# Performance work log

Measured on AMD Instinct MI355X. Metric: run time of the kernel, lower is better.

## Reference

```python
import jax, jax.numpy as jnp
import numpy as np

B, T, D, U_DIM = 256, 512, 256, 256


def setup_inputs() -> dict:
    key = jax.random.key(0)
    k_x, k_len, k_w, k_u, k_b = jax.random.split(key, 5)
    codes = jax.random.normal(k_x, (B, T, D), dtype=jnp.float32)
    # random valid lengths; zero the tail so Masking(mask_value=0) kicks in
    lengths = jax.random.randint(k_len, (B,), T // 2, T + 1)
    valid = (jnp.arange(T)[None, :] < lengths[:, None]).astype(jnp.float32)
    codes = codes * valid[:, :, None]
    # Keras GRU params (reset_after=True): kernel, recurrent_kernel, bias[2, 3U]
    s_in = 1.0 / np.sqrt(D)
    s_rec = 1.0 / np.sqrt(U_DIM)
    W = jax.random.uniform(k_w, (D, 3 * U_DIM), jnp.float32, -s_in, s_in)
    Uk = jax.random.uniform(k_u, (U_DIM, 3 * U_DIM), jnp.float32, -s_rec, s_rec)
    b = jax.random.uniform(k_b, (2, 3 * U_DIM), jnp.float32, -s_rec, s_rec)
    return {"codes": codes, "W": W, "Uk": Uk, "b": b}


def _gru_scan(codes, W, Uk, b):
    units = Uk.shape[0]
    # Masking(mask_value=0): timestep is masked if ALL features equal 0
    mask = jnp.any(codes != 0.0, axis=-1)  # [B, T] bool
    # Precompute input projections for all timesteps: [B, T, 3U]
    mat_x = jnp.einsum("btd,dk->btk", codes, W) + b[0]
    xs = (jnp.swapaxes(mat_x, 0, 1), jnp.swapaxes(mask, 0, 1))  # time-major
    h0 = jnp.zeros((codes.shape[0], units), dtype=codes.dtype)

    def step(h, inp):
        mx_t, m_t = inp  # [B, 3U], [B]
        mh_t = h @ Uk + b[1]  # [B, 3U]
        xz, xr, xh = jnp.split(mx_t, 3, axis=-1)
        hz, hr, hh = jnp.split(mh_t, 3, axis=-1)
        z = jax.nn.sigmoid(xz + hz)
        r = jax.nn.sigmoid(xr + hr)
        h_cand = jnp.tanh(xh + r * hh)
        h_new = z * h + (1.0 - z) * h_cand
        h_out = jnp.where(m_t[:, None], h_new, h)  # carry state on masked steps
        return h_out, None

    h_final, _ = jax.lax.scan(step, h0, xs)
    return h_final  # [B, units]


def reference(codes, W, Uk, b):
    return _gru_scan(codes, W, Uk, b)
```

## Files before the change

### kernel.cpp

```cpp
#include <hip/hip_runtime.h>
#include <hip/hip_bf16.h>
#include <cstdint>
#include <cstddef>

#define Bb 256
#define Tt 512
#define Dd 256
#define Uu 256
#define NJ 768

#define WS_MASK  1024
#define WS_UKP   132096
#define WS_MATX  525312

typedef _Float16 h2 __attribute__((ext_vector_type(2)));
typedef short short8 __attribute__((ext_vector_type(8)));
typedef float f32x4 __attribute__((ext_vector_type(4)));

#if defined(__has_builtin)
#if __has_builtin(__builtin_amdgcn_fdot2)
#define HAVE_FDOT2 1
#endif
#endif

__device__ __forceinline__ unsigned int pack2(float a, float b) {
    h2 v;
    v.x = (_Float16)a;
    v.y = (_Float16)b;
    return __builtin_bit_cast(unsigned int, v);
}

__device__ __forceinline__ float dot2_acc(unsigned int u, unsigned int hv, float acc) {
    h2 a = __builtin_bit_cast(h2, u);
    h2 b = __builtin_bit_cast(h2, hv);
#ifdef HAVE_FDOT2
    return __builtin_amdgcn_fdot2(a, b, acc, false);
#else
    return acc + (float)a.x * (float)b.x + (float)a.y * (float)b.y;
#endif
}

__device__ __forceinline__ void bfsplit(float x, unsigned short& h, unsigned short& l) {
    unsigned u = __builtin_bit_cast(unsigned, x);
    h = (unsigned short)(u >> 16);
    float hf = __builtin_bit_cast(float, u & 0xFFFF0000u);
    float lf = x - hf;
    l = (unsigned short)(__builtin_bit_cast(unsigned, lf) >> 16);
}

union PK8 { unsigned short s[8]; uint4 v; };

__global__ void zero_len_kernel(int* __restrict__ len) {
    if (threadIdx.x < Bb) len[threadIdx.x] = 0;
}

__global__ void mask_len_kernel(const float* __restrict__ codes,
                                unsigned char* __restrict__ mask,
                                int* __restrict__ len) {
    const int wave = threadIdx.x >> 6;
    const int lane = threadIdx.x & 63;
    const long long row = (long long)blockIdx.x * 4 + wave;
    const float4* p = reinterpret_cast<const float4*>(codes + row * Dd);
    float4 v = p[lane];
    bool nz = (v.x != 0.f) || (v.y != 0.f) || (v.z != 0.f) || (v.w != 0.f);
    unsigned long long ball = __ballot(nz);
    if (lane == 0) {
        int b = (int)(row >> 9);
        int t = (int)(row & 511);
        unsigned char m = (ball != 0ull) ? 1 : 0;
        mask[row] = m;
        if (m) atomicMax(&len[b], t + 1);
    }
}

__global__ void uk_convert_kernel(const float* __restrict__ Uk,
                                  unsigned int* __restrict__ ukp) {
    int idx = blockIdx.x * 256 + threadIdx.x;
    int col = idx & 255;
    int kp = (idx >> 8) & 127;
    int g = idx >> 15;
    float a = Uk[(size_t)(2 * kp) * NJ + (g << 8) + col];
    float b = Uk[(size_t)(2 * kp + 1) * NJ + (g << 8) + col];
    ukp[idx] = pack2(a, b);
}

__global__ __launch_bounds__(256, 2)
void matx_gemm_mfma(const float* __restrict__ codes,
                    const float* __restrict__ W,
                    const float* __restrict__ b0,
                    float* __restrict__ matx,
                    int t0, int ctShift) {
    __shared__ uint4 AH[1024], AL[1024], BH[1024], BL[1024];
    const int tid = threadIdx.x;
    const int w = tid >> 6, lane = tid & 63;
    const int rbase = blockIdx.x * 128, cbase = blockIdx.y * 128;
    const int ctMask = (1 << ctShift) - 1;

    f32x4 acc[4][4];
#pragma unroll
    for (int i = 0; i < 4; ++i)
#pragma unroll
        for (int j = 0; j < 4; ++j) acc[i][j] = (f32x4){0.f, 0.f, 0.f, 0.f};

    const int cB = tid & 127, kqB = tid >> 7;

    for (int kt = 0; kt < 4; ++kt) {
        const int k0 = kt * 64;
#pragma unroll
        for (int u = 0; u < 4; ++u) {
            int L = u * 256 + tid;
            int r = L >> 3, o = L & 7;
            int gr = rbase + r;
            size_t g = (size_t)(gr >> ctShift) * Tt + (size_t)(t0 + (gr & ctMask));
            const float* cp = codes + g * Dd + k0 + (o << 3);
            float4 f0 = *reinterpret_cast<const float4*>(cp);
            float4 f1 = *reinterpret_cast<const float4*>(cp + 4);
            float e[8] = {f0.x, f0.y, f0.z, f0.w, f1.x, f1.y, f1.z, f1.w};
            PK8 hp, lp;
#pragma unroll
            for (int i = 0; i < 8; ++i) bfsplit(e[i], hp.s[i], lp.s[i]);
            int idx = (((o >> 2) * 8 + (r >> 4)) << 6) + ((r & 15) | ((o & 3) << 4));
            AH[idx] = hp.v;
            AL[idx] = lp.v;
        }
        {
            PK8 ph[4], pl[4];
#pragma unroll
            for (int j = 0; j < 32; ++j) {
                float v = W[(size_t)(k0 + kqB * 32 + j) * NJ + cbase + cB];
                bfsplit(v, ph[j >> 3].s[j & 7], pl[j >> 3].s[j & 7]);
            }
#pragma unroll
            for (int o2 = 0; o2 < 4; ++o2) {
                int idx = ((kqB * 8 + (cB >> 4)) << 6) + ((cB & 15) | (o2 << 4));
                BH[idx] = ph[o2].v;
                BL[idx] = pl[o2].v;
            }
        }
        __syncthreads();
        const int mbase = (w & 1) * 4, nbase = (w >> 1) * 4;
#pragma unroll
        for (int ki = 0; ki < 2; ++ki) {
            short8 ah[4], al2[4], bh[4], bl2[4];
#pragma unroll
            for (int x = 0; x < 4; ++x) {
                ah[x]  = *reinterpret_cast<const short8*>(&AH[((ki * 8 + mbase + x) << 6) + lane]);
                al2[x] = *reinterpret_cast<const short8*>(&AL[((ki * 8 + mbase + x) << 6) + lane]);
                bh[x]  = *reinterpret_cast<const short8*>(&BH[((ki * 8 + nbase + x) << 6) + lane]);
                bl2[x] = *reinterpret_cast<const short8*>(&BL[((ki * 8 + nbase + x) << 6) + lane]);
            }
#pragma unroll
            for (int mi = 0; mi < 4; ++mi)
#pragma unroll
                for (int ni = 0; ni < 4; ++ni) {
                    acc[mi][ni] = __builtin_amdgcn_mfma_f32_16x16x32_bf16(ah[mi], bh[ni], acc[mi][ni], 0, 0, 0);
                    acc[mi][ni] = __builtin_amdgcn_mfma_f32_16x16x32_bf16(ah[mi], bl2[ni], acc[mi][ni], 0, 0, 0);
                    acc[mi][ni] = __builtin_amdgcn_mfma_f32_16x16x32_bf16(al2[mi], bh[ni], acc[mi][ni], 0, 0, 0);
                }
        }
        __syncthreads();
    }
    const int colq = lane & 15, rowq = (lane >> 4) * 4;
#pragma unroll
    for (int ni = 0; ni < 4; ++ni) {
        int cc = cbase + (w >> 1) * 64 + ni * 16 + colq;
        float bv = b0[cc];
#pragma unroll
        for (int mi = 0; mi < 4; ++mi) {
            int gr = rbase + (w & 1) * 64 + mi * 16 + rowq;
#pragma unroll
            for (int j = 0; j < 4; ++j)
                matx[(size_t)(gr + j) * NJ + cc] = acc[mi][ni][j] + bv;
        }
    }
}

__global__ __launch_bounds__(512, 2)
void gru_scan_kernel(const float* __restrict__ matx,
                     const unsigned int* __restrict__ ukp,
                     const float* __restrict__ bias1,
                     const unsigned char* __restrict__ mask,
                     const int* __restrict__ len,
                     float* __restrict__ out,
                     int t0, int CT) {
    __shared__ __align__(16) unsigned int hH[128];
    __shared__ float part[2][3][Uu];

    const int tid = threadIdx.x;
    const int b = blockIdx.x;
    const int col = tid & 255;
    const int khalf = tid >> 8;

    unsigned int ukz[64], ukr[64], ukh[64];
    {
        const unsigned int* u0 = ukp + (khalf << 14) + col;
#pragma unroll
        for (int i = 0; i < 64; ++i) ukz[i] = u0[i << 8];
        const unsigned int* u1 = u0 + (128 << 8);
#pragma unroll
        for (int i = 0; i < 64; ++i) ukr[i] = u1[i << 8];
        const unsigned int* u2 = u1 + (128 << 8);
#pragma unroll
        for (int i = 0; i < 64; ++i) ukh[i] = u2[i << 8];
    }
#pragma unroll
    for (int i = 0; i < 64; ++i) {
        asm volatile("" : "+v"(ukz[i]), "+v"(ukr[i]), "+v"(ukh[i]));
    }

    int S = len[b] - t0;
    S = S < 0 ? 0 : (S > CT ? CT : S);

    float hprev = 0.f, bz = 0.f, br = 0.f, bh = 0.f;
    if (tid < 256) {
        hprev = (t0 == 0) ? 0.f : out[(size_t)b * Uu + col];
        bz = bias1[col];
        br = bias1[col + 256];
        bh = bias1[col + 512];
    }
    if (tid < 128) {
        float e0 = 0.f, e1 = 0.f;
        if (t0 != 0) {
            e0 = out[(size_t)b * Uu + 2 * tid];
            e1 = out[(size_t)b * Uu + 2 * tid + 1];
        }
        hH[tid] = pack2(e0, e1);
    }
    __syncthreads();

    const unsigned char* mrow_mask = mask + (size_t)b * Tt + t0;
    for (int s = 0; s < S; ++s) {
        float mxz = 0.f, mxr = 0.f, mxh = 0.f;
        unsigned char m = 0;
        if (tid < 256) {
            const float* mrow = matx + ((size_t)b * CT + s) * NJ;
            mxz = mrow[col];
            mxr = mrow[col + 256];
            mxh = mrow[col + 512];
            m = mrow_mask[s];
        }

        float az = 0.f, ar = 0.f, ah = 0.f;
        const unsigned int* hp = &hH[khalf << 6];
#pragma unroll
        for (int i = 0; i < 16; ++i) {
            uint4 q = *reinterpret_cast<const uint4*>(hp + (i << 2));
            az = dot2_acc(ukz[4 * i + 0], q.x, az);
            ar = dot2_acc(ukr[4 * i + 0], q.x, ar);
            ah = dot2_acc(ukh[4 * i + 0], q.x, ah);
            az = dot2_acc(ukz[4 * i + 1], q.y, az);
            ar = dot2_acc(ukr[4 * i + 1], q.y, ar);
            ah = dot2_acc(ukh[4 * i + 1], q.y, ah);
            az = dot2_acc(ukz[4 * i + 2], q.z, az);
            ar = dot2_acc(ukr[4 * i + 2], q.z, ar);
            ah = dot2_acc(ukh[4 * i + 2], q.z, ah);
            az = dot2_acc(ukz[4 * i + 3], q.w, az);
            ar = dot2_acc(ukr[4 * i + 3], q.w, ar);
            ah = dot2_acc(ukh[4 * i + 3], q.w, ah);
        }
        part[khalf][0][col] = az;
        part[khalf][1][col] = ar;
        part[khalf][2][col] = ah;
        __syncthreads();

        if (tid < 256) {
            float azs = part[0][0][col] + part[1][0][col];
            float ars = part[0][1][col] + part[1][1][col];
            float ahs = part[0][2][col] + part[1][2][col];
            float hn = hprev;
            if (m) {
                float z = 1.f / (1.f + expf(-(mxz + azs + bz)));
                float r = 1.f / (1.f + expf(-(mxr + ars + br)));
                float hc = tanhf(mxh + r * (ahs + bh));
                hn = z * hprev + (1.f - z) * hc;
            }
            hprev = hn;
            float ho = __shfl_xor(hn, 1);
            if (!(col & 1)) hH[col >> 1] = pack2(hn, ho);
        }
        __syncthreads();
    }

    if (tid < 256) out[(size_t)b * Uu + col] = hprev;
}

extern "C" void kernel_launch(void* const* d_in, const int* in_sizes, int n_in,
                              void* d_out, int out_size, void* d_ws, size_t ws_size,
                              hipStream_t stream) {
    const float* codes = (const float*)d_in[0];
    const float* W     = (const float*)d_in[1];
    const float* Uk    = (const float*)d_in[2];
    const float* bias  = (const float*)d_in[3];
    float* out = (float*)d_out;

    char* ws = (char*)d_ws;
    int* len = (int*)ws;
    unsigned char* mask = (unsigned char*)(ws + WS_MASK);
    unsigned int* ukp = (unsigned int*)(ws + WS_UKP);
    float* matx = (float*)(ws + WS_MATX);

    int CT = 1;
    for (int cc = 512; cc >= 1; cc >>= 1) {
        if ((size_t)WS_MATX + (size_t)cc * 786432ull <= ws_size) { CT = cc; break; }
    }
    int ctShift = __builtin_ctz((unsigned)CT);
    int nch = 512 / CT;

    zero_len_kernel<<<1, 256, 0, stream>>>(len);
    mask_len_kernel<<<Bb * Tt / 4, 256, 0, stream>>>(codes, mask, len);
    uk_convert_kernel<<<384, 256, 0, stream>>>(Uk, ukp);

    for (int c = 0; c < nch; ++c) {
        int t0 = c * CT;
        dim3 grid(2 * CT, 6);
        matx_gemm_mfma<<<grid, 256, 0, stream>>>(codes, W, bias, matx, t0, ctShift);
        gru_scan_kernel<<<Bb, 512, 0, stream>>>(matx, ukp, bias + NJ, mask, len,
                                                out, t0, CT);
    }
}
```

Before: 1.446 ms.

## Pre-split codes and W into MFMA fragment layout and drop LDS from GEMM

Adds separate kernels that split codes and W into bf16 hi/lo pairs once and store them in the MFMA fragment order. The GEMM then loads fragments straight from global memory into registers with double buffering, so it no longer stages through LDS or needs barriers. The asm register pin in the scan is moved inside the time loop, and the minimum chunk size is raised to 128. The cost is an extra large workspace (about 135 MB) and an extra pass over codes in the split kernel.

```diff
diff --git a/kernel.cpp b/kernel.cpp
--- a/kernel.cpp
+++ b/kernel.cpp
@@ -11,7 +11,11 @@
 
 #define WS_MASK  1024
 #define WS_UKP   132096
-#define WS_MATX  525312
+#define WS_WH    525312
+#define WS_WL    918528
+#define WS_CH    1311744
+#define WS_CL    68420608
+#define WS_MATX  135529472ull
 
 typedef _Float16 h2 __attribute__((ext_vector_type(2)));
 typedef short short8 __attribute__((ext_vector_type(8)));
@@ -84,17 +88,64 @@
     ukp[idx] = pack2(a, b);
 }
 
+__global__ void wsplit_kernel(const float* __restrict__ W,
+                              uint4* __restrict__ WH4, uint4* __restrict__ WL4) {
+    int T = blockIdx.x * 256 + threadIdx.x;
+    int lane = T & 63, nsub = (T >> 6) & 7, ki = (T >> 9) & 7, cs = T >> 12;
+    int n = cs * 128 + nsub * 16 + (lane & 15);
+    int k0 = ki * 32 + ((lane >> 4) & 3) * 8;
+    PK8 hp, lp;
+#pragma unroll
+    for (int e = 0; e < 8; ++e) bfsplit(W[(size_t)(k0 + e) * NJ + n], hp.s[e], lp.s[e]);
+    WH4[T] = hp.v;
+    WL4[T] = lp.v;
+}
+
+__global__ void csplit_kernel(const float* __restrict__ codes,
+                              uint4* __restrict__ CH4, uint4* __restrict__ CL4) {
+    int T = blockIdx.x * 256 + threadIdx.x;
+    int lane = T & 63, rsub = (T >> 6) & 7, ki = (T >> 9) & 7, tile = T >> 12;
+    size_t row = (size_t)tile * 128 + rsub * 16 + (lane & 15);
+    int k0 = ki * 32 + ((lane >> 4) & 3) * 8;
+    const float* cp = codes + row * Dd + k0;
+    float4 f0 = *reinterpret_cast<const float4*>(cp);
+    float4 f1 = *reinterpret_cast<const float4*>(cp + 4);
+    float e[8] = {f0.x, f0.y, f0.z, f0.w, f1.x, f1.y, f1.z, f1.w};
+    PK8 hp, lp;
+#pragma unroll
+    for (int i = 0; i < 8; ++i) bfsplit(e[i], hp.s[i], lp.s[i]);
+    CH4[T] = hp.v;
+    CL4[T] = lp.v;
+}
+
+#define LOADF(buf, kig)                                                        \
+    do {                                                                       \
+        _Pragma("unroll") for (int x = 0; x < 4; ++x) {                        \
+            ah[buf][x] = Ahp[(kig) * 512 + x * 64];                            \
+            al[buf][x] = Alp[(kig) * 512 + x * 64];                            \
+            bh[buf][x] = Bhp[(kig) * 512 + x * 64];                            \
+            bl[buf][x] = Blp[(kig) * 512 + x * 64];                            \
+        }                                                                      \
+    } while (0)
+
 __global__ __launch_bounds__(256, 2)
-void matx_gemm_mfma(const float* __restrict__ codes,
-                    const float* __restrict__ W,
-                    const float* __restrict__ b0,
-                    float* __restrict__ matx,
-                    int t0, int ctShift) {
-    __shared__ uint4 AH[1024], AL[1024], BH[1024], BL[1024];
+void matx_gemm_reg(const uint4* __restrict__ CH4, const uint4* __restrict__ CL4,
+                   const uint4* __restrict__ WH4, const uint4* __restrict__ WL4,
+                   const float* __restrict__ b0, float* __restrict__ matx,
+                   int t0, int ctShift) {
     const int tid = threadIdx.x;
     const int w = tid >> 6, lane = tid & 63;
-    const int rbase = blockIdx.x * 128, cbase = blockIdx.y * 128;
+    const int mbase = (w & 1) * 4, nbase = (w >> 1) * 4;
+    const int cs = blockIdx.y;
+    const int rbase = blockIdx.x * 128;
     const int ctMask = (1 << ctShift) - 1;
+    const size_t grow0 = (size_t)(rbase >> ctShift) * Tt + (size_t)(t0 + (rbase & ctMask));
+    const size_t gtile = grow0 >> 7;
+
+    const uint4* Ahp = CH4 + gtile * 4096 + mbase * 64 + lane;
+    const uint4* Alp = CL4 + gtile * 4096 + mbase * 64 + lane;
+    const uint4* Bhp = WH4 + (size_t)cs * 4096 + nbase * 64 + lane;
+    const uint4* Blp = WL4 + (size_t)cs * 4096 + nbase * 64 + lane;
 
     f32x4 acc[4][4];
 #pragma unroll
@@ -102,65 +153,28 @@
 #pragma unroll
         for (int j = 0; j < 4; ++j) acc[i][j] = (f32x4){0.f, 0.f, 0.f, 0.f};
 
-    const int cB = tid & 127, kqB = tid >> 7;
-
-    for (int kt = 0; kt < 4; ++kt) {
-        const int k0 = kt * 64;
-#pragma unroll
-        for (int u = 0; u < 4; ++u) {
-            int L = u * 256 + tid;
-            int r = L >> 3, o = L & 7;
-            int gr = rbase + r;
-            size_t g = (size_t)(gr >> ctShift) * Tt + (size_t)(t0 + (gr & ctMask));
-            const float* cp = codes + g * Dd + k0 + (o << 3);
-            float4 f0 = *reinterpret_cast<const float4*>(cp);
-            float4 f1 = *reinterpret_cast<const float4*>(cp + 4);
-            float e[8] = {f0.x, f0.y, f0.z, f0.w, f1.x, f1.y, f1.z, f1.w};
-            PK8 hp, lp;
-#pragma unroll
-            for (int i = 0; i < 8; ++i) bfsplit(e[i], hp.s[i], lp.s[i]);
-            int idx = (((o >> 2) * 8 + (r >> 4)) << 6) + ((r & 15) | ((o & 3) << 4));
-            AH[idx] = hp.v;
-            AL[idx] = lp.v;
-        }
-        {
-            PK8 ph[4], pl[4];
-#pragma unroll
-            for (int j = 0; j < 32; ++j) {
-                float v = W[(size_t)(k0 + kqB * 32 + j) * NJ + cbase + cB];
-                bfsplit(v, ph[j >> 3].s[j & 7], pl[j >> 3].s[j & 7]);
+    uint4 ah[2][4], al[2][4], bh[2][4], bl[2][4];
+    LOADF(0, 0);
+#pragma unroll
+    for (int kig = 0; kig < 8; ++kig) {
+        const int cur = kig & 1, nx = cur ^ 1;
+        if (kig < 7) LOADF(nx, kig + 1);
+#pragma unroll
+        for (int mi = 0; mi < 4; ++mi) {
+            short8 am = __builtin_bit_cast(short8, ah[cur][mi]);
+            short8 al8 = __builtin_bit_cast(short8, al[cur][mi]);
+#pragma unroll
+            for (int ni = 0; ni < 4; ++ni) {
+                short8 bn = __builtin_bit_cast(short8, bh[cur][ni]);
+                short8 bl8 = __builtin_bit_cast(short8, bl[cur][ni]);
+                acc[mi][ni] = __builtin_amdgcn_mfma_f32_16x16x32_bf16(am, bn, acc[mi][ni], 0, 0, 0);
+                acc[mi][ni] = __builtin_amdgcn_mfma_f32_16x16x32_bf16(am, bl8, acc[mi][ni], 0, 0, 0);
+                acc[mi][ni] = __builtin_amdgcn_mfma_f32_16x16x32_bf16(al8, bn, acc[mi][ni], 0, 0, 0);
             }
-#pragma unroll
-            for (int o2 = 0; o2 < 4; ++o2) {
-                int idx = ((kqB * 8 + (cB >> 4)) << 6) + ((cB & 15) | (o2 << 4));
-                BH[idx] = ph[o2].v;
-                BL[idx] = pl[o2].v;
-            }
-        }
-        __syncthreads();
-        const int mbase = (w & 1) * 4, nbase = (w >> 1) * 4;
-#pragma unroll
-        for (int ki = 0; ki < 2; ++ki) {
-            short8 ah[4], al2[4], bh[4], bl2[4];
-#pragma unroll
-            for (int x = 0; x < 4; ++x) {
-                ah[x]  = *reinterpret_cast<const short8*>(&AH[((ki * 8 + mbase + x) << 6) + lane]);
-                al2[x] = *reinterpret_cast<const short8*>(&AL[((ki * 8 + mbase + x) << 6) + lane]);
-                bh[x]  = *reinterpret_cast<const short8*>(&BH[((ki * 8 + nbase + x) << 6) + lane]);
-                bl2[x] = *reinterpret_cast<const short8*>(&BL[((ki * 8 + nbase + x) << 6) + lane]);
-            }
-#pragma unroll
-            for (int mi = 0; mi < 4; ++mi)
-#pragma unroll
-                for (int ni = 0; ni < 4; ++ni) {
-                    acc[mi][ni] = __builtin_amdgcn_mfma_f32_16x16x32_bf16(ah[mi], bh[ni], acc[mi][ni], 0, 0, 0);
-                    acc[mi][ni] = __builtin_amdgcn_mfma_f32_16x16x32_bf16(ah[mi], bl2[ni], acc[mi][ni], 0, 0, 0);
-                    acc[mi][ni] = __builtin_amdgcn_mfma_f32_16x16x32_bf16(al2[mi], bh[ni], acc[mi][ni], 0, 0, 0);
-                }
-        }
-        __syncthreads();
+        }
     }
     const int colq = lane & 15, rowq = (lane >> 4) * 4;
+    const int cbase = cs * 128;
 #pragma unroll
     for (int ni = 0; ni < 4; ++ni) {
         int cc = cbase + (w >> 1) * 64 + ni * 16 + colq;
@@ -203,10 +217,6 @@
 #pragma unroll
         for (int i = 0; i < 64; ++i) ukh[i] = u2[i << 8];
     }
-#pragma unroll
-    for (int i = 0; i < 64; ++i) {
-        asm volatile("" : "+v"(ukz[i]), "+v"(ukr[i]), "+v"(ukh[i]));
-    }
 
     int S = len[b] - t0;
     S = S < 0 ? 0 : (S > CT ? CT : S);
@@ -230,6 +240,10 @@
 
     const unsigned char* mrow_mask = mask + (size_t)b * Tt + t0;
     for (int s = 0; s < S; ++s) {
+#pragma unroll
+        for (int i = 0; i < 64; ++i) {
+            asm volatile("" : "+v"(ukz[i]), "+v"(ukr[i]), "+v"(ukh[i]));
+        }
         float mxz = 0.f, mxr = 0.f, mxh = 0.f;
         unsigned char m = 0;
         if (tid < 256) {
@@ -297,11 +311,15 @@
     int* len = (int*)ws;
     unsigned char* mask = (unsigned char*)(ws + WS_MASK);
     unsigned int* ukp = (unsigned int*)(ws + WS_UKP);
+    uint4* WH4 = (uint4*)(ws + WS_WH);
+    uint4* WL4 = (uint4*)(ws + WS_WL);
+    uint4* CH4 = (uint4*)(ws + WS_CH);
+    uint4* CL4 = (uint4*)(ws + WS_CL);
     float* matx = (float*)(ws + WS_MATX);
 
-    int CT = 1;
-    for (int cc = 512; cc >= 1; cc >>= 1) {
-        if ((size_t)WS_MATX + (size_t)cc * 786432ull <= ws_size) { CT = cc; break; }
+    int CT = 128;
+    for (int cc = 512; cc >= 128; cc >>= 1) {
+        if (WS_MATX + (size_t)cc * 786432ull <= ws_size) { CT = cc; break; }
     }
     int ctShift = __builtin_ctz((unsigned)CT);
     int nch = 512 / CT;
@@ -309,11 +327,14 @@
     zero_len_kernel<<<1, 256, 0, stream>>>(len);
     mask_len_kernel<<<Bb * Tt / 4, 256, 0, stream>>>(codes, mask, len);
     uk_convert_kernel<<<384, 256, 0, stream>>>(Uk, ukp);
+    wsplit_kernel<<<96, 256, 0, stream>>>(W, WH4, WL4);
+    csplit_kernel<<<16384, 256, 0, stream>>>(codes, CH4, CL4);
 
     for (int c = 0; c < nch; ++c) {
         int t0 = c * CT;
         dim3 grid(2 * CT, 6);
-        matx_gemm_mfma<<<grid, 256, 0, stream>>>(codes, W, bias, matx, t0, ctShift);
+        matx_gemm_reg<<<grid, 256, 0, stream>>>(CH4, CL4, WH4, WL4, bias, matx,
+                                                t0, ctShift);
         gru_scan_kernel<<<Bb, 512, 0, stream>>>(matx, ukp, bias + NJ, mask, len,
                                                 out, t0, CT);
     }
```

New measurement: 1.416 ms. 2.1% less time.

## Pre-split W into bf16 MFMA layout and store matx as fp16

Applied to the files above, without the earlier changes.

W is split once into hi/lo bf16 fragments laid out in MFMA order, so the GEMM loads B operands straight into registers instead of converting through shared memory each tile. The input-projection buffer matx is written and read as fp16, halving its traffic between the GEMM and the scan kernels. The register-pinning asm barrier moves inside the scan loop, and the minimum chunk size is raised to 128. Storing the projections in fp16 adds rounding error to the GRU inputs.

```diff
diff --git a/kernel.cpp b/kernel.cpp
--- a/kernel.cpp
+++ b/kernel.cpp
@@ -11,7 +11,9 @@
 
 #define WS_MASK  1024
 #define WS_UKP   132096
-#define WS_MATX  525312
+#define WS_WH    525312
+#define WS_WL    918528
+#define WS_MATX  1311744ull
 
 typedef _Float16 h2 __attribute__((ext_vector_type(2)));
 typedef short short8 __attribute__((ext_vector_type(8)));
@@ -84,17 +86,31 @@
     ukp[idx] = pack2(a, b);
 }
 
+__global__ void wsplit_kernel(const float* __restrict__ W,
+                              uint4* __restrict__ WH4, uint4* __restrict__ WL4) {
+    int T = blockIdx.x * 256 + threadIdx.x;
+    int lane = T & 63, nsub = (T >> 6) & 7, ki = (T >> 9) & 7, cs = T >> 12;
+    int n = cs * 128 + nsub * 16 + (lane & 15);
+    int k0 = ki * 32 + ((lane >> 4) & 3) * 8;
+    PK8 hp, lp;
+#pragma unroll
+    for (int e = 0; e < 8; ++e) bfsplit(W[(size_t)(k0 + e) * NJ + n], hp.s[e], lp.s[e]);
+    WH4[T] = hp.v;
+    WL4[T] = lp.v;
+}
+
 __global__ __launch_bounds__(256, 2)
-void matx_gemm_mfma(const float* __restrict__ codes,
-                    const float* __restrict__ W,
-                    const float* __restrict__ b0,
-                    float* __restrict__ matx,
+void matx_gemm_half(const float* __restrict__ codes,
+                    const uint4* __restrict__ WH4, const uint4* __restrict__ WL4,
+                    const float* __restrict__ b0, _Float16* __restrict__ matx,
                     int t0, int ctShift) {
-    __shared__ uint4 AH[1024], AL[1024], BH[1024], BL[1024];
+    __shared__ uint4 AH[1024], AL[1024];
     const int tid = threadIdx.x;
     const int w = tid >> 6, lane = tid & 63;
-    const int rbase = blockIdx.x * 128, cbase = blockIdx.y * 128;
+    const int rbase = blockIdx.x * 128;
+    const int cs = blockIdx.y;
     const int ctMask = (1 << ctShift) - 1;
+    const int mbase = (w & 1) * 4, nbase = (w >> 1) * 4;
 
     f32x4 acc[4][4];
 #pragma unroll
@@ -102,10 +118,20 @@
 #pragma unroll
         for (int j = 0; j < 4; ++j) acc[i][j] = (f32x4){0.f, 0.f, 0.f, 0.f};
 
-    const int cB = tid & 127, kqB = tid >> 7;
+    const uint4* Bh0 = WH4 + (size_t)cs * 4096 + nbase * 64 + lane;
+    const uint4* Bl0 = WL4 + (size_t)cs * 4096 + nbase * 64 + lane;
 
     for (int kt = 0; kt < 4; ++kt) {
         const int k0 = kt * 64;
+        uint4 bhv[2][4], blv[2][4];
+#pragma unroll
+        for (int ki2 = 0; ki2 < 2; ++ki2)
+#pragma unroll
+            for (int x = 0; x < 4; ++x) {
+                bhv[ki2][x] = Bh0[(kt * 2 + ki2) * 512 + x * 64];
+                blv[ki2][x] = Bl0[(kt * 2 + ki2) * 512 + x * 64];
+            }
+        if (kt > 0) __syncthreads();
 #pragma unroll
         for (int u = 0; u < 4; ++u) {
             int L = u * 256 + tid;
@@ -123,44 +149,29 @@
             AH[idx] = hp.v;
             AL[idx] = lp.v;
         }
-        {
-            PK8 ph[4], pl[4];
-#pragma unroll
-            for (int j = 0; j < 32; ++j) {
-                float v = W[(size_t)(k0 + kqB * 32 + j) * NJ + cbase + cB];
-                bfsplit(v, ph[j >> 3].s[j & 7], pl[j >> 3].s[j & 7]);
+        __syncthreads();
+#pragma unroll
+        for (int ki2 = 0; ki2 < 2; ++ki2) {
+            short8 ah[4], al8[4];
+#pragma unroll
+            for (int x = 0; x < 4; ++x) {
+                ah[x]  = *reinterpret_cast<const short8*>(&AH[((ki2 * 8 + mbase + x) << 6) + lane]);
+                al8[x] = *reinterpret_cast<const short8*>(&AL[((ki2 * 8 + mbase + x) << 6) + lane]);
             }
 #pragma unroll
-            for (int o2 = 0; o2 < 4; ++o2) {
-                int idx = ((kqB * 8 + (cB >> 4)) << 6) + ((cB & 15) | (o2 << 4));
-                BH[idx] = ph[o2].v;
-                BL[idx] = pl[o2].v;
-            }
-        }
-        __syncthreads();
-        const int mbase = (w & 1) * 4, nbase = (w >> 1) * 4;
-#pragma unroll
-        for (int ki = 0; ki < 2; ++ki) {
-            short8 ah[4], al2[4], bh[4], bl2[4];
-#pragma unroll
-            for (int x = 0; x < 4; ++x) {
-                ah[x]  = *reinterpret_cast<const short8*>(&AH[((ki * 8 + mbase + x) << 6) + lane]);
-                al2[x] = *reinterpret_cast<const short8*>(&AL[((ki * 8 + mbase + x) << 6) + lane]);
-                bh[x]  = *reinterpret_cast<const short8*>(&BH[((ki * 8 + nbase + x) << 6) + lane]);
-                bl2[x] = *reinterpret_cast<const short8*>(&BL[((ki * 8 + nbase + x) << 6) + lane]);
-            }
-#pragma unroll
             for (int mi = 0; mi < 4; ++mi)
 #pragma unroll
                 for (int ni = 0; ni < 4; ++ni) {
-                    acc[mi][ni] = __builtin_amdgcn_mfma_f32_16x16x32_bf16(ah[mi], bh[ni], acc[mi][ni], 0, 0, 0);
-                    acc[mi][ni] = __builtin_amdgcn_mfma_f32_16x16x32_bf16(ah[mi], bl2[ni], acc[mi][ni], 0, 0, 0);
-                    acc[mi][ni] = __builtin_amdgcn_mfma_f32_16x16x32_bf16(al2[mi], bh[ni], acc[mi][ni], 0, 0, 0);
+                    short8 bn  = __builtin_bit_cast(short8, bhv[ki2][ni]);
+                    short8 bl8 = __builtin_bit_cast(short8, blv[ki2][ni]);
+                    acc[mi][ni] = __builtin_amdgcn_mfma_f32_16x16x32_bf16(ah[mi], bn, acc[mi][ni], 0, 0, 0);
+                    acc[mi][ni] = __builtin_amdgcn_mfma_f32_16x16x32_bf16(ah[mi], bl8, acc[mi][ni], 0, 0, 0);
+                    acc[mi][ni] = __builtin_amdgcn_mfma_f32_16x16x32_bf16(al8[mi], bn, acc[mi][ni], 0, 0, 0);
                 }
         }
-        __syncthreads();
     }
     const int colq = lane & 15, rowq = (lane >> 4) * 4;
+    const int cbase = cs * 128;
 #pragma unroll
     for (int ni = 0; ni < 4; ++ni) {
         int cc = cbase + (w >> 1) * 64 + ni * 16 + colq;
@@ -170,13 +181,13 @@
             int gr = rbase + (w & 1) * 64 + mi * 16 + rowq;
 #pragma unroll
             for (int j = 0; j < 4; ++j)
-                matx[(size_t)(gr + j) * NJ + cc] = acc[mi][ni][j] + bv;
+                matx[(size_t)(gr + j) * NJ + cc] = (_Float16)(acc[mi][ni][j] + bv);
         }
     }
 }
 
 __global__ __launch_bounds__(512, 2)
-void gru_scan_kernel(const float* __restrict__ matx,
+void gru_scan_kernel(const _Float16* __restrict__ matx,
                      const unsigned int* __restrict__ ukp,
                      const float* __restrict__ bias1,
                      const unsigned char* __restrict__ mask,
@@ -203,10 +214,6 @@
 #pragma unroll
         for (int i = 0; i < 64; ++i) ukh[i] = u2[i << 8];
     }
-#pragma unroll
-    for (int i = 0; i < 64; ++i) {
-        asm volatile("" : "+v"(ukz[i]), "+v"(ukr[i]), "+v"(ukh[i]));
-    }
 
     int S = len[b] - t0;
     S = S < 0 ? 0 : (S > CT ? CT : S);
@@ -230,13 +237,17 @@
 
     const unsigned char* mrow_mask = mask + (size_t)b * Tt + t0;
     for (int s = 0; s < S; ++s) {
+#pragma unroll
+        for (int i = 0; i < 64; ++i) {
+            asm volatile("" : "+v"(ukz[i]), "+v"(ukr[i]), "+v"(ukh[i]));
+        }
         float mxz = 0.f, mxr = 0.f, mxh = 0.f;
         unsigned char m = 0;
         if (tid < 256) {
-            const float* mrow = matx + ((size_t)b * CT + s) * NJ;
-            mxz = mrow[col];
-            mxr = mrow[col + 256];
-            mxh = mrow[col + 512];
+            const _Float16* mrow = matx + ((size_t)b * CT + s) * NJ;
+            mxz = (float)mrow[col];
+            mxr = (float)mrow[col + 256];
+            mxh = (float)mrow[col + 512];
             m = mrow_mask[s];
         }
 
@@ -297,11 +308,13 @@
     int* len = (int*)ws;
     unsigned char* mask = (unsigned char*)(ws + WS_MASK);
     unsigned int* ukp = (unsigned int*)(ws + WS_UKP);
-    float* matx = (float*)(ws + WS_MATX);
-
-    int CT = 1;
-    for (int cc = 512; cc >= 1; cc >>= 1) {
-        if ((size_t)WS_MATX + (size_t)cc * 786432ull <= ws_size) { CT = cc; break; }
+    uint4* WH4 = (uint4*)(ws + WS_WH);
+    uint4* WL4 = (uint4*)(ws + WS_WL);
+    _Float16* matx = (_Float16*)(ws + WS_MATX);
+
+    int CT = 128;
+    for (int cc = 512; cc >= 128; cc >>= 1) {
+        if (WS_MATX + (size_t)cc * 393216ull <= ws_size) { CT = cc; break; }
     }
     int ctShift = __builtin_ctz((unsigned)CT);
     int nch = 512 / CT;
@@ -309,11 +322,13 @@
     zero_len_kernel<<<1, 256, 0, stream>>>(len);
     mask_len_kernel<<<Bb * Tt / 4, 256, 0, stream>>>(codes, mask, len);
     uk_convert_kernel<<<384, 256, 0, stream>>>(Uk, ukp);
+    wsplit_kernel<<<96, 256, 0, stream>>>(W, WH4, WL4);
 
     for (int c = 0; c < nch; ++c) {
         int t0 = c * CT;
         dim3 grid(2 * CT, 6);
-        matx_gemm_mfma<<<grid, 256, 0, stream>>>(codes, W, bias, matx, t0, ctShift);
+        matx_gemm_half<<<grid, 256, 0, stream>>>(codes, WH4, WL4, bias, matx,
+                                                 t0, ctShift);
         gru_scan_kernel<<<Bb, 512, 0, stream>>>(matx, ukp, bias + NJ, mask, len,
                                                 out, t0, CT);
     }
```

After: 1.375 ms. -4.9%, faster.
